# Optimization experiments

Hardware: AMD Instinct MI355X
Metric: run time of the kernel (lower is better)

The kernel has to match this reference:

```python
import jax, jax.numpy as jnp
import numpy as np

B, S, DIN, DOUT = 2, 2048, 4096, 4096


def setup_inputs() -> dict:
    key = jax.random.key(0)
    k1, k2 = jax.random.split(key)
    x = jax.random.normal(k1, (B, S, DIN), dtype=jnp.float32)
    weight = jax.random.normal(k2, (DOUT, DIN), dtype=jnp.float32) * 0.02
    # xnor init for row scaling pattern
    mean = weight.mean(-1, keepdims=True)                      # [DOUT,1]
    scale = jnp.abs(weight - mean).mean(-1, keepdims=True)     # [DOUT,1]
    wscale = scale
    wbias = mean
    return {"x": x, "weight": weight, "wscale": wscale, "wbias": wbias}


def reference(x, weight, wscale, wbias):
    # STE binarization: forward = sign(weight) (grad handled in bwd module)
    w_bin = jnp.sign(weight)
    w = wscale * w_bin + wbias                                 # [DOUT, DIN]
    # F.linear(x, w): x @ w.T, no bias
    out = jnp.einsum('bsk,nk->bsn', x, w)
    return out
```

## Files before the change

kernel.cpp:

```cpp
#include <hip/hip_runtime.h>
#include <stdint.h>


#define MDIM 4096
#define NDIM 4096
#define KDIM 4096

typedef int   int4v  __attribute__((ext_vector_type(4)));

__device__ __forceinline__ int pack4_rn(float a, float b, float c, float d, float inv) {
  int ia = __float2int_rn(a * inv) & 0xff;
  int ib = __float2int_rn(b * inv) & 0xff;
  int ic = __float2int_rn(c * inv) & 0xff;
  int id = __float2int_rn(d * inv) & 0xff;
  return ia | (ib << 8) | (ic << 16) | (id << 24);
}

__device__ __forceinline__ int sgn8(float v) {
  return (v > 0.f) ? 1 : ((v < 0.f) ? 0xff : 0);
}

__global__ __launch_bounds__(256) void quant_x_kernel(
    const float* __restrict__ x, char* __restrict__ xq,
    float* __restrict__ xscale, float* __restrict__ sumx) {
  const int row = blockIdx.x;
  const int tid = threadIdx.x;
  const float4* xr = (const float4*)(x + (size_t)row * KDIM);
  float4 v[4];
  float s = 0.f, amax = 0.f;
#pragma unroll
  for (int u = 0; u < 4; ++u) {
    v[u] = xr[u * 256 + tid];
    s += v[u].x + v[u].y + v[u].z + v[u].w;
    amax = fmaxf(amax, fmaxf(fmaxf(fabsf(v[u].x), fabsf(v[u].y)),
                             fmaxf(fabsf(v[u].z), fabsf(v[u].w))));
  }
#pragma unroll
  for (int off = 32; off > 0; off >>= 1) {
    s += __shfl_down(s, off, 64);
    amax = fmaxf(amax, __shfl_down(amax, off, 64));
  }
  __shared__ float rs[4], rm[4], bcast;
  if ((tid & 63) == 0) { rs[tid >> 6] = s; rm[tid >> 6] = amax; }
  __syncthreads();
  if (tid == 0) {
    sumx[row] = rs[0] + rs[1] + rs[2] + rs[3];
    float mt = fmaxf(fmaxf(rm[0], rm[1]), fmaxf(rm[2], rm[3]));
    xscale[row] = mt * (1.f / 127.f);
    bcast = (mt > 0.f) ? 127.f / mt : 0.f;
  }
  __syncthreads();
  const float inv = bcast;
  int* xo = (int*)(xq + (size_t)row * KDIM);
#pragma unroll
  for (int u = 0; u < 4; ++u)
    xo[u * 256 + tid] = pack4_rn(v[u].x, v[u].y, v[u].z, v[u].w, inv);
}

__global__ __launch_bounds__(256) void sign_w_kernel(
    const float* __restrict__ w, char* __restrict__ wsg) {
  const size_t base = (size_t)blockIdx.x * (256 * 4);
  const float4* wr = (const float4*)w;
  int* wo = (int*)wsg;
#pragma unroll
  for (int u = 0; u < 4; ++u) {
    size_t i = base + u * 256 + threadIdx.x;
    float4 v = wr[i];
    wo[i] = sgn8(v.x) | (sgn8(v.y) << 8) | (sgn8(v.z) << 16) | (sgn8(v.w) << 24);
  }
}

__global__ __launch_bounds__(256) void gemm_bin_i8_kernel(
    const char* __restrict__ A,
    const char* __restrict__ Bs,
    const float* __restrict__ wscale, const float* __restrict__ wbias,
    const float* __restrict__ xscale, const float* __restrict__ sumx,
    float* __restrict__ C) {
  __shared__ __align__(16) char sA[128 * 128];
  __shared__ __align__(16) char sB[128 * 128];

  const int bn = blockIdx.x & 31;
  const int bm = blockIdx.x >> 5;
  const int tm0 = bm * 128, tn0 = bn * 128;
  const int tid = threadIdx.x;
  const int lane = tid & 63, wave = tid >> 6;
  const int quad = lane >> 4, l16 = lane & 15;
  const int wmo = (wave >> 1) * 64, wno = (wave & 1) * 64;

  int4v acc[4][4];
  const int4v zero4 = {0, 0, 0, 0};
#pragma unroll
  for (int i = 0; i < 4; ++i)
#pragma unroll
    for (int j = 0; j < 4; ++j) acc[i][j] = zero4;

  int st_row[4], st_lblk[4];
#pragma unroll
  for (int q = 0; q < 4; ++q) {
    int u = q * 256 + tid;
    int row = u >> 3, pblk = u & 7;
    st_row[q] = row;
    st_lblk[q] = pblk ^ (row & 7);
  }

  int aOff[4][2], bOff[4][2];
#pragma unroll
  for (int i = 0; i < 4; ++i) {
    int r = wmo + i * 16 + l16;
#pragma unroll
    for (int s = 0; s < 2; ++s)
      aOff[i][s] = r * 128 + ((s * 4 + quad) ^ (r & 7)) * 16;
  }
#pragma unroll
  for (int j = 0; j < 4; ++j) {
    int r = wno + j * 16 + l16;
#pragma unroll
    for (int s = 0; s < 2; ++s)
      bOff[j][s] = r * 128 + ((s * 4 + quad) ^ (r & 7)) * 16;
  }

  for (int kt = 0; kt < KDIM; kt += 128) {
#pragma unroll
    for (int q = 0; q < 4; ++q) {
      const char* ga = A  + (size_t)(tm0 + st_row[q]) * KDIM + kt + st_lblk[q] * 16;
      const char* gb = Bs + (size_t)(tn0 + st_row[q]) * KDIM + kt + st_lblk[q] * 16;
      char* la = sA + (q * 256 + tid) * 16;
      char* lb = sB + (q * 256 + tid) * 16;
      __builtin_amdgcn_global_load_lds(
          (const __attribute__((address_space(1))) void*)ga,
          (__attribute__((address_space(3))) void*)la, 16, 0, 0);
      __builtin_amdgcn_global_load_lds(
          (const __attribute__((address_space(1))) void*)gb,
          (__attribute__((address_space(3))) void*)lb, 16, 0, 0);
    }
    __syncthreads();

#pragma unroll
    for (int s = 0; s < 2; ++s) {
      int4v af[4], bfr[4];
#pragma unroll
      for (int i = 0; i < 4; ++i) af[i] = *(const int4v*)(sA + aOff[i][s]);
#pragma unroll
      for (int j = 0; j < 4; ++j) bfr[j] = *(const int4v*)(sB + bOff[j][s]);
#pragma unroll
      for (int i = 0; i < 4; ++i)
#pragma unroll
        for (int j = 0; j < 4; ++j)
          acc[i][j] = __builtin_amdgcn_mfma_i32_16x16x64_i8(af[i], bfr[j], acc[i][j], 0, 0, 0);
    }

    __syncthreads();
  }

  float wsv[4], wbv[4];
#pragma unroll
  for (int j = 0; j < 4; ++j) {
    int n = tn0 + wno + j * 16 + l16;
    wsv[j] = wscale[n];
    wbv[j] = wbias[n];
  }
#pragma unroll
  for (int i = 0; i < 4; ++i) {
#pragma unroll
    for (int r = 0; r < 4; ++r) {
      int m = tm0 + wmo + i * 16 + quad * 4 + r;
      float xs = xscale[m];
      float sx = sumx[m];
      float* crow = C + (size_t)m * NDIM + tn0 + wno + l16;
#pragma unroll
      for (int j = 0; j < 4; ++j) {
        crow[j * 16] = wsv[j] * xs * (float)acc[i][j][r] + wbv[j] * sx;
      }
    }
  }
}

extern "C" void kernel_launch(void* const* d_in, const int* in_sizes, int n_in,
                              void* d_out, int out_size, void* d_ws, size_t ws_size,
                              hipStream_t stream) {
  const float* x      = (const float*)d_in[0];
  const float* weight = (const float*)d_in[1];
  const float* wscale = (const float*)d_in[2];
  const float* wbias  = (const float*)d_in[3];
  float* out = (float*)d_out;

  char* xq  = (char*)d_ws;
  char* wsg = xq + (size_t)MDIM * KDIM;
  float* xscale = (float*)(wsg + (size_t)NDIM * KDIM);
  float* sumx   = xscale + MDIM;

  quant_x_kernel<<<MDIM, 256, 0, stream>>>(x, xq, xscale, sumx);
  sign_w_kernel<<<((size_t)NDIM * KDIM) / (16 * 256), 256, 0, stream>>>(weight, wsg);
  gemm_bin_i8_kernel<<<(MDIM / 128) * (NDIM / 128), 256, 0, stream>>>(
      xq, wsg, wscale, wbias, xscale, sumx, out);
}
```

Measured before the change: 247.4 us.

## Double-buffer GEMM K-tiles in LDS and merge prep kernels into one launch

The GEMM main loop now splits each 128-wide K step into two 64-wide LDS buffers. The load for the next half is issued before computing on the current one, so global-to-LDS transfers overlap the MFMA work, and there is one barrier per half instead of two per step. The LDS swizzle is adapted to 64-byte rows. The x-quantization and weight-sign kernels are fused into a single launch that branches on block index, removing one kernel launch and letting the two preprocessing passes run concurrently. The risk is that the overlap depends on the compiler not inserting conservative waits on the async LDS loads.

Measured after the change: 248.1 us. Within noise of the previous version (+0.3%).

```diff
diff --git a/kernel.cpp b/kernel.cpp
--- a/kernel.cpp
+++ b/kernel.cpp
@@ -6,7 +6,7 @@
 #define NDIM 4096
 #define KDIM 4096
 
-typedef int   int4v  __attribute__((ext_vector_type(4)));
+typedef int int4v __attribute__((ext_vector_type(4)));
 
 __device__ __forceinline__ int pack4_rn(float a, float b, float c, float d, float inv) {
   int ia = __float2int_rn(a * inv) & 0xff;
@@ -20,64 +20,64 @@
   return (v > 0.f) ? 1 : ((v < 0.f) ? 0xff : 0);
 }
 
-__global__ __launch_bounds__(256) void quant_x_kernel(
-    const float* __restrict__ x, char* __restrict__ xq,
+__global__ __launch_bounds__(256) void prep_kernel(
+    const float* __restrict__ x, const float* __restrict__ w,
+    char* __restrict__ xq, char* __restrict__ wsg,
     float* __restrict__ xscale, float* __restrict__ sumx) {
-  const int row = blockIdx.x;
+  const int b = blockIdx.x;
   const int tid = threadIdx.x;
-  const float4* xr = (const float4*)(x + (size_t)row * KDIM);
-  float4 v[4];
-  float s = 0.f, amax = 0.f;
-#pragma unroll
-  for (int u = 0; u < 4; ++u) {
-    v[u] = xr[u * 256 + tid];
-    s += v[u].x + v[u].y + v[u].z + v[u].w;
-    amax = fmaxf(amax, fmaxf(fmaxf(fabsf(v[u].x), fabsf(v[u].y)),
-                             fmaxf(fabsf(v[u].z), fabsf(v[u].w))));
-  }
-#pragma unroll
-  for (int off = 32; off > 0; off >>= 1) {
-    s += __shfl_down(s, off, 64);
-    amax = fmaxf(amax, __shfl_down(amax, off, 64));
-  }
-  __shared__ float rs[4], rm[4], bcast;
-  if ((tid & 63) == 0) { rs[tid >> 6] = s; rm[tid >> 6] = amax; }
-  __syncthreads();
-  if (tid == 0) {
-    sumx[row] = rs[0] + rs[1] + rs[2] + rs[3];
-    float mt = fmaxf(fmaxf(rm[0], rm[1]), fmaxf(rm[2], rm[3]));
-    xscale[row] = mt * (1.f / 127.f);
-    bcast = (mt > 0.f) ? 127.f / mt : 0.f;
-  }
-  __syncthreads();
-  const float inv = bcast;
-  int* xo = (int*)(xq + (size_t)row * KDIM);
-#pragma unroll
-  for (int u = 0; u < 4; ++u)
-    xo[u * 256 + tid] = pack4_rn(v[u].x, v[u].y, v[u].z, v[u].w, inv);
-}
-
-__global__ __launch_bounds__(256) void sign_w_kernel(
-    const float* __restrict__ w, char* __restrict__ wsg) {
-  const size_t base = (size_t)blockIdx.x * (256 * 4);
-  const float4* wr = (const float4*)w;
-  int* wo = (int*)wsg;
-#pragma unroll
-  for (int u = 0; u < 4; ++u) {
-    size_t i = base + u * 256 + threadIdx.x;
-    float4 v = wr[i];
-    wo[i] = sgn8(v.x) | (sgn8(v.y) << 8) | (sgn8(v.z) << 16) | (sgn8(v.w) << 24);
+  if (b < MDIM) {
+    const int row = b;
+    const float4* xr = (const float4*)(x + (size_t)row * KDIM);
+    float4 v[4];
+    float s = 0.f, amax = 0.f;
+#pragma unroll
+    for (int u = 0; u < 4; ++u) {
+      v[u] = xr[u * 256 + tid];
+      s += v[u].x + v[u].y + v[u].z + v[u].w;
+      amax = fmaxf(amax, fmaxf(fmaxf(fabsf(v[u].x), fabsf(v[u].y)),
+                               fmaxf(fabsf(v[u].z), fabsf(v[u].w))));
+    }
+#pragma unroll
+    for (int off = 32; off > 0; off >>= 1) {
+      s += __shfl_down(s, off, 64);
+      amax = fmaxf(amax, __shfl_down(amax, off, 64));
+    }
+    __shared__ float rs[4], rm[4], bcast;
+    if ((tid & 63) == 0) { rs[tid >> 6] = s; rm[tid >> 6] = amax; }
+    __syncthreads();
+    if (tid == 0) {
+      sumx[row] = rs[0] + rs[1] + rs[2] + rs[3];
+      float mt = fmaxf(fmaxf(rm[0], rm[1]), fmaxf(rm[2], rm[3]));
+      xscale[row] = mt * (1.f / 127.f);
+      bcast = (mt > 0.f) ? 127.f / mt : 0.f;
+    }
+    __syncthreads();
+    const float inv = bcast;
+    int* xo = (int*)(xq + (size_t)row * KDIM);
+#pragma unroll
+    for (int u = 0; u < 4; ++u)
+      xo[u * 256 + tid] = pack4_rn(v[u].x, v[u].y, v[u].z, v[u].w, inv);
+  } else {
+    const size_t base = (size_t)(b - MDIM) * (256 * 4);
+    const float4* wr = (const float4*)w;
+    int* wo = (int*)wsg;
+#pragma unroll
+    for (int u = 0; u < 4; ++u) {
+      size_t i = base + u * 256 + tid;
+      float4 v = wr[i];
+      wo[i] = sgn8(v.x) | (sgn8(v.y) << 8) | (sgn8(v.z) << 16) | (sgn8(v.w) << 24);
+    }
   }
 }
 
 __global__ __launch_bounds__(256) void gemm_bin_i8_kernel(
-    const char* __restrict__ A,
-    const char* __restrict__ Bs,
+    const char* __restrict__ A, const char* __restrict__ Bs,
     const float* __restrict__ wscale, const float* __restrict__ wbias,
     const float* __restrict__ xscale, const float* __restrict__ sumx,
     float* __restrict__ C) {
-  __shared__ __align__(16) char sA[128 * 128];
-  __shared__ __align__(16) char sB[128 * 128];
+  __shared__ __align__(16) char sA0[128 * 64], sA1[128 * 64];
+  __shared__ __align__(16) char sB0[128 * 64], sB1[128 * 64];
 
   const int bn = blockIdx.x & 31;
   const int bm = blockIdx.x >> 5;
@@ -94,63 +94,71 @@
 #pragma unroll
     for (int j = 0; j < 4; ++j) acc[i][j] = zero4;
 
-  int st_row[4], st_lblk[4];
-#pragma unroll
-  for (int q = 0; q < 4; ++q) {
+  int st_row[2], st_lblk[2];
+#pragma unroll
+  for (int q = 0; q < 2; ++q) {
     int u = q * 256 + tid;
-    int row = u >> 3, pblk = u & 7;
-    st_row[q] = row;
-    st_lblk[q] = pblk ^ (row & 7);
-  }
-
-  int aOff[4][2], bOff[4][2];
+    st_row[q] = u >> 2;
+    st_lblk[q] = (u & 3) ^ ((st_row[q] >> 1) & 3);
+  }
+  const char* gA0 = A  + (size_t)(tm0 + st_row[0]) * KDIM + st_lblk[0] * 16;
+  const char* gA1 = A  + (size_t)(tm0 + st_row[1]) * KDIM + st_lblk[1] * 16;
+  const char* gB0 = Bs + (size_t)(tn0 + st_row[0]) * KDIM + st_lblk[0] * 16;
+  const char* gB1 = Bs + (size_t)(tn0 + st_row[1]) * KDIM + st_lblk[1] * 16;
+  const int ld0 = tid * 16, ld1 = 4096 + tid * 16;
+
+  int aOff[4], bOff[4];
 #pragma unroll
   for (int i = 0; i < 4; ++i) {
     int r = wmo + i * 16 + l16;
-#pragma unroll
-    for (int s = 0; s < 2; ++s)
-      aOff[i][s] = r * 128 + ((s * 4 + quad) ^ (r & 7)) * 16;
+    aOff[i] = r * 64 + (quad ^ ((r >> 1) & 3)) * 16;
   }
 #pragma unroll
   for (int j = 0; j < 4; ++j) {
     int r = wno + j * 16 + l16;
-#pragma unroll
-    for (int s = 0; s < 2; ++s)
-      bOff[j][s] = r * 128 + ((s * 4 + quad) ^ (r & 7)) * 16;
-  }
-
+    bOff[j] = r * 64 + (quad ^ ((r >> 1) & 3)) * 16;
+  }
+
+#define STAGE(dstA, dstB, kofs)                                                  \
+  do {                                                                           \
+    __builtin_amdgcn_global_load_lds(                                            \
+        (const __attribute__((address_space(1))) void*)(gA0 + (kofs)),           \
+        (__attribute__((address_space(3))) void*)((dstA) + ld0), 16, 0, 0);      \
+    __builtin_amdgcn_global_load_lds(                                            \
+        (const __attribute__((address_space(1))) void*)(gA1 + (kofs)),           \
+        (__attribute__((address_space(3))) void*)((dstA) + ld1), 16, 0, 0);      \
+    __builtin_amdgcn_global_load_lds(                                            \
+        (const __attribute__((address_space(1))) void*)(gB0 + (kofs)),           \
+        (__attribute__((address_space(3))) void*)((dstB) + ld0), 16, 0, 0);      \
+    __builtin_amdgcn_global_load_lds(                                            \
+        (const __attribute__((address_space(1))) void*)(gB1 + (kofs)),           \
+        (__attribute__((address_space(3))) void*)((dstB) + ld1), 16, 0, 0);      \
+  } while (0)
+
+#define COMPUTE(srcA, srcB)                                                      \
+  do {                                                                           \
+    int4v af[4], bfr[4];                                                         \
+    _Pragma("unroll") for (int i = 0; i < 4; ++i)                                \
+        af[i] = *(const int4v*)((srcA) + aOff[i]);                               \
+    _Pragma("unroll") for (int j = 0; j < 4; ++j)                                \
+        bfr[j] = *(const int4v*)((srcB) + bOff[j]);                              \
+    _Pragma("unroll") for (int i = 0; i < 4; ++i)                                \
+        _Pragma("unroll") for (int j = 0; j < 4; ++j)                            \
+            acc[i][j] = __builtin_amdgcn_mfma_i32_16x16x64_i8(af[i], bfr[j],     \
+                                                              acc[i][j], 0, 0, 0);\
+  } while (0)
+
+  STAGE(sA0, sB0, 0);
   for (int kt = 0; kt < KDIM; kt += 128) {
-#pragma unroll
-    for (int q = 0; q < 4; ++q) {
-      const char* ga = A  + (size_t)(tm0 + st_row[q]) * KDIM + kt + st_lblk[q] * 16;
-      const char* gb = Bs + (size_t)(tn0 + st_row[q]) * KDIM + kt + st_lblk[q] * 16;
-      char* la = sA + (q * 256 + tid) * 16;
-      char* lb = sB + (q * 256 + tid) * 16;
-      __builtin_amdgcn_global_load_lds(
-          (const __attribute__((address_space(1))) void*)ga,
-          (__attribute__((address_space(3))) void*)la, 16, 0, 0);
-      __builtin_amdgcn_global_load_lds(
-          (const __attribute__((address_space(1))) void*)gb,
-          (__attribute__((address_space(3))) void*)lb, 16, 0, 0);
-    }
-    __syncthreads();
-
-#pragma unroll
-    for (int s = 0; s < 2; ++s) {
-      int4v af[4], bfr[4];
-#pragma unroll
-      for (int i = 0; i < 4; ++i) af[i] = *(const int4v*)(sA + aOff[i][s]);
-#pragma unroll
-      for (int j = 0; j < 4; ++j) bfr[j] = *(const int4v*)(sB + bOff[j][s]);
-#pragma unroll
-      for (int i = 0; i < 4; ++i)
-#pragma unroll
-        for (int j = 0; j < 4; ++j)
-          acc[i][j] = __builtin_amdgcn_mfma_i32_16x16x64_i8(af[i], bfr[j], acc[i][j], 0, 0, 0);
-    }
-
-    __syncthreads();
-  }
+    __syncthreads();
+    if (kt + 64 < KDIM) STAGE(sA1, sB1, kt + 64);
+    COMPUTE(sA0, sB0);
+    __syncthreads();
+    if (kt + 128 < KDIM) STAGE(sA0, sB0, kt + 128);
+    COMPUTE(sA1, sB1);
+  }
+#undef STAGE
+#undef COMPUTE
 
   float wsv[4], wbv[4];
 #pragma unroll
@@ -189,8 +197,8 @@
   float* xscale = (float*)(wsg + (size_t)NDIM * KDIM);
   float* sumx   = xscale + MDIM;
 
-  quant_x_kernel<<<MDIM, 256, 0, stream>>>(x, xq, xscale, sumx);
-  sign_w_kernel<<<((size_t)NDIM * KDIM) / (16 * 256), 256, 0, stream>>>(weight, wsg);
+  prep_kernel<<<MDIM + (NDIM * KDIM) / (16 * 256), 256, 0, stream>>>(
+      x, weight, xq, wsg, xscale, sumx);
   gemm_bin_i8_kernel<<<(MDIM / 128) * (NDIM / 128), 256, 0, stream>>>(
       xq, wsg, wscale, wbias, xscale, sumx, out);
 }
```
